# Optimization experiments

Measured on AMD Instinct MI355X. Metric: run time of the kernel, lower is better.

The kernel has to match this reference:

```python
import jax, jax.numpy as jnp
import numpy as np

NHEAD = 16
HEAD_DIM = 64
ROPE_BASE = 10000.0


def _rotate_half(x):
    # interleaved convention: pairs (x0,x1)->(-x1,x0)
    x1 = x[..., ::2]
    x2 = x[..., 1::2]
    return jnp.stack([-x2, x1], axis=-1).reshape(x.shape)


def _rope_cache(seq_len, head_dim, base):
    half = head_dim // 2
    inv_freq = 1.0 / base ** (jnp.arange(half, dtype=jnp.float32) / float(half))
    t = jnp.arange(seq_len, dtype=jnp.float32)
    freqs = jnp.einsum('i,j->ij', t, inv_freq)          # [T, half]
    emb = jnp.concatenate([freqs, freqs], axis=-1)      # [T, D] (half-half cat, matches torch source)
    return jnp.cos(emb), jnp.sin(emb)


def setup_inputs() -> dict:
    key = jax.random.key(0)
    k1, k2, k3 = jax.random.split(key, 3)
    b, t, c = 2, 2048, 1024
    x = jax.random.normal(k1, (b, t, c), dtype=jnp.float32)
    # torch nn.Linear weights: [out_features, in_features], scaled like kaiming-uniform-ish
    W_qkv = jax.random.normal(k2, (3 * c, c), dtype=jnp.float32) / np.sqrt(c)
    W_out = jax.random.normal(k3, (c, c), dtype=jnp.float32) / np.sqrt(c)
    return {"x": x, "W_qkv": W_qkv, "W_out": W_out}


def reference(x, W_qkv, W_out):
    b, t, c = x.shape
    nh, hd = NHEAD, HEAD_DIM
    qkv = x @ W_qkv.T                                   # [b, t, 3c]
    q, k, v = jnp.split(qkv, 3, axis=-1)

    def to_heads(a):
        return a.reshape(b, t, nh, hd).transpose(0, 2, 1, 3)  # [b, nh, t, hd]

    q, k, v = to_heads(q), to_heads(k), to_heads(v)
    cos, sin = _rope_cache(t, hd, ROPE_BASE)            # [t, hd]
    cos = cos.astype(q.dtype)[None, None]
    sin = sin.astype(q.dtype)[None, None]
    q = q * cos + _rotate_half(q) * sin
    k = k * cos + _rotate_half(k) * sin

    scale = 1.0 / np.sqrt(hd).astype(np.float32)
    scores = jnp.einsum('bhqd,bhkd->bhqk', q, k) * scale
    attn = jax.nn.softmax(scores, axis=-1)
    y = jnp.einsum('bhqk,bhkd->bhqd', attn, v)          # [b, nh, t, hd]
    y = y.transpose(0, 2, 1, 3).reshape(b, t, c)
    return y @ W_out.T
```

## Files before the change

### kernel.cpp

```cpp
#include <hip/hip_runtime.h>
#include <hip/hip_bf16.h>
#include <math.h>

typedef __hip_bfloat16 bf16;
typedef _Float16 f16;
typedef __attribute__((ext_vector_type(8))) short bf16x8;
typedef __attribute__((ext_vector_type(8))) _Float16 f16x8;
typedef __attribute__((ext_vector_type(4))) float f32x4;

#define MFMA_BF(a,b,c) __builtin_amdgcn_mfma_f32_16x16x32_bf16((a),(b),(c),0,0,0)
#define MFMA_F16(a,b,c) __builtin_amdgcn_mfma_f32_16x16x32_f16((a),(b),(c),0,0,0)

__device__ __forceinline__ void load_lds16(const void* g, void* l) {
  __builtin_amdgcn_global_load_lds(
      (__attribute__((address_space(1))) void*)(g),
      (__attribute__((address_space(3))) void*)(l), 16, 0, 0);
}

__device__ __forceinline__ unsigned pk_bf16(float a, float b) {
  unsigned ua = __builtin_bit_cast(unsigned, a);
  unsigned ub = __builtin_bit_cast(unsigned, b);
  ua += 0x7fffu + ((ua >> 16) & 1u);
  ub += 0x7fffu + ((ub >> 16) & 1u);
  return (ua >> 16) | (ub & 0xffff0000u);
}

__global__ void cvt_all(const float* __restrict__ x, const float* __restrict__ wq,
                        const float* __restrict__ wo, unsigned* __restrict__ xb,
                        unsigned* __restrict__ wqb, unsigned* __restrict__ wob) {
  int i = blockIdx.x * blockDim.x + threadIdx.x;
  const float* src;
  unsigned* dst;
  int off;
  if (i < 1048576) { src = x; dst = xb; off = i; }
  else if (i < 1048576 + 786432) { src = wq; dst = wqb; off = i - 1048576; }
  else { src = wo; dst = wob; off = i - (1048576 + 786432); }
  float4 v = reinterpret_cast<const float4*>(src)[off];
  uint2 u;
  u.x = pk_bf16(v.x, v.y);
  u.y = pk_bf16(v.z, v.w);
  reinterpret_cast<uint2*>(dst)[off] = u;
}

__global__ __launch_bounds__(256, 2)
void gemm_qkv(const bf16* __restrict__ A, const bf16* __restrict__ B,
              bf16* __restrict__ outq, bf16* __restrict__ outk,
              f16* __restrict__ outv) {
  __shared__ __align__(16) bf16 As[128 * 32];
  __shared__ __align__(16) bf16 Bs[128 * 32];
  __shared__ __align__(16) f16 Ts[4][32 * 72];
  const int K = 1024;
  const int tid = threadIdx.x;
  const int w = tid >> 6;
  const int lane = tid & 63;
  const int quad = lane >> 4;
  const int col = lane & 15;
  const int waveM = w >> 1;
  const int waveN = w & 1;
  const int bm = blockIdx.y * 128;
  const int bn = blockIdx.x * 128;

  f32x4 acc[4][4] = {};
  const int srow = lane >> 2;
  const int skoff = (lane & 3) * 8;

  for (int k0 = 0; k0 < K; k0 += 32) {
    __syncthreads();
#pragma unroll
    for (int p = 0; p < 2; ++p) {
      int r = p * 64 + w * 16 + srow;
      load_lds16(A + (size_t)(bm + r) * K + k0 + skoff, (char*)As + p * 4096 + w * 1024);
      load_lds16(B + (size_t)(bn + r) * K + k0 + skoff, (char*)Bs + p * 4096 + w * 1024);
    }
    __syncthreads();
    bf16x8 af[4], bfr[4];
#pragma unroll
    for (int i = 0; i < 4; ++i)
      af[i] = *reinterpret_cast<const bf16x8*>(As + (waveM * 64 + i * 16 + col) * 32 + quad * 8);
#pragma unroll
    for (int j = 0; j < 4; ++j)
      bfr[j] = *reinterpret_cast<const bf16x8*>(Bs + (waveN * 64 + j * 16 + col) * 32 + quad * 8);
#pragma unroll
    for (int i = 0; i < 4; ++i)
#pragma unroll
      for (int j = 0; j < 4; ++j)
        acc[i][j] = MFMA_BF(af[i], bfr[j], acc[i][j]);
  }

  if (bn < 2048) {
    const float NEGK = -0.4152410118f;
    const float C1 = 0.1803368799f;
    const float sgn = (col & 1) ? 1.0f : -1.0f;
#pragma unroll
    for (int j = 0; j < 4; ++j) {
      const int n0 = bn + waveN * 64 + j * 16;
      const int sel = n0 >> 10;
      const int hh = (n0 & 1023) >> 6;
      const int dd = (n0 & 63) + col;
      bf16* outp = sel ? outk : outq;
      const float post = sel ? 1.0f : C1;
      const float invf = __builtin_amdgcn_exp2f((float)((n0 & 31) + col) * NEGK);
#pragma unroll
      for (int i = 0; i < 4; ++i) {
#pragma unroll
        for (int r = 0; r < 4; ++r) {
          int m = bm + waveM * 64 + i * 16 + quad * 4 + r;
          int b = m >> 11, t = m & 2047;
          float v = acc[i][j][r];
          float partner = __shfl_xor(v, 1);
          float ang = (float)t * invf;
          float res = (v * __cosf(ang) + sgn * partner * __sinf(ang)) * post;
          outp[((size_t)(b * 16 + hh) * 2048 + t) * 64 + dd] = __float2bfloat16(res);
        }
      }
    }
  } else {
    f16* tb = &Ts[w][0];
    const int nq = bn + waveN * 64;
    const int hh = (nq & 1023) >> 6;
    const int b = bm >> 11;
    const int tbase = (bm & 2047) + waveM * 64;
    f16* dst0 = outv + (size_t)(b * 16 + hh) * 64 * 2048;
#pragma unroll
    for (int jh = 0; jh < 2; ++jh) {
#pragma unroll
      for (int j2 = 0; j2 < 2; ++j2) {
        const int j = jh * 2 + j2;
        const int dl = j2 * 16 + col;
#pragma unroll
        for (int i = 0; i < 4; ++i)
#pragma unroll
          for (int r = 0; r < 4; ++r)
            tb[dl * 72 + i * 16 + quad * 4 + r] = (f16)acc[i][j][r];
      }
      __asm__ volatile("s_waitcnt lgkmcnt(0)" ::: "memory");
      const int dl = lane >> 1;
      const int thalf = (lane & 1) * 32;
#pragma unroll
      for (int rr = 0; rr < 4; ++rr) {
        f16x8 vrow = *reinterpret_cast<const f16x8*>(tb + dl * 72 + thalf + rr * 8);
        *reinterpret_cast<f16x8*>(dst0 + (size_t)(jh * 32 + dl) * 2048 + tbase + thalf + rr * 8) = vrow;
      }
      __asm__ volatile("s_waitcnt lgkmcnt(0)" ::: "memory");
    }
  }
}

__global__ __launch_bounds__(256, 2)
void gemm_out(const bf16* __restrict__ A, const bf16* __restrict__ B,
              float* __restrict__ outf) {
  __shared__ __align__(16) bf16 As[64 * 32];
  __shared__ __align__(16) bf16 Bs[128 * 32];
  const int K = 1024;
  const int tid = threadIdx.x;
  const int w = tid >> 6;
  const int lane = tid & 63;
  const int quad = lane >> 4;
  const int col = lane & 15;
  const int bm = blockIdx.y * 64;
  const int bn = blockIdx.x * 128;

  f32x4 acc[4][2] = {};
  const int srow = lane >> 2;
  const int skoff = (lane & 3) * 8;

  for (int k0 = 0; k0 < K; k0 += 32) {
    __syncthreads();
    load_lds16(A + (size_t)(bm + w * 16 + srow) * K + k0 + skoff, (char*)As + w * 1024);
#pragma unroll
    for (int p = 0; p < 2; ++p)
      load_lds16(B + (size_t)(bn + p * 64 + w * 16 + srow) * K + k0 + skoff,
                 (char*)Bs + p * 4096 + w * 1024);
    __syncthreads();
    bf16x8 af[4], bfr[2];
#pragma unroll
    for (int i = 0; i < 4; ++i)
      af[i] = *reinterpret_cast<const bf16x8*>(As + (i * 16 + col) * 32 + quad * 8);
#pragma unroll
    for (int j = 0; j < 2; ++j)
      bfr[j] = *reinterpret_cast<const bf16x8*>(Bs + (w * 32 + j * 16 + col) * 32 + quad * 8);
#pragma unroll
    for (int i = 0; i < 4; ++i)
#pragma unroll
      for (int j = 0; j < 2; ++j)
        acc[i][j] = MFMA_BF(af[i], bfr[j], acc[i][j]);
  }

#pragma unroll
  for (int i = 0; i < 4; ++i)
#pragma unroll
    for (int j = 0; j < 2; ++j) {
      const int n0 = bn + w * 32 + j * 16;
#pragma unroll
      for (int r = 0; r < 4; ++r) {
        int m = bm + i * 16 + quad * 4 + r;
        outf[(size_t)m * 1024 + n0 + col] = acc[i][j][r];
      }
    }
}

__global__ __launch_bounds__(256, 2)
void attn_kernel(const bf16* __restrict__ qh, const bf16* __restrict__ kh,
                 const f16* __restrict__ vt, bf16* __restrict__ y) {
  __shared__ __align__(16) bf16 Ks[2][64 * 64];
  __shared__ __align__(16) f16 Vs[2][64 * 64];
  __shared__ __align__(16) f16 Ps[4][32 * 72];

  const int bh = blockIdx.y;
  const int w = threadIdx.x >> 6;
  const int lane = threadIdx.x & 63;
  const int quad = lane >> 4;
  const int col = lane & 15;

  const int qrow0 = blockIdx.x * 128 + w * 32 + col;
  bf16x8 qf[2][2];
#pragma unroll
  for (int f = 0; f < 2; ++f)
#pragma unroll
    for (int c = 0; c < 2; ++c)
      qf[f][c] = *reinterpret_cast<const bf16x8*>(
          qh + ((size_t)bh * 2048 + qrow0 + f * 16) * 64 + c * 32 + quad * 8);

  const int s8 = lane >> 3;
  const int blk = (lane & 7) ^ s8;
  const bf16* kg = kh + (size_t)bh * 2048 * 64;
  const f16* vg = vt + (size_t)bh * 64 * 2048;
  char* klds0 = (char*)&Ks[0][0] + w * 2048;
  char* vlds0 = (char*)&Vs[0][0] + w * 2048;
  const int ksrc0 = s8 * 4 + w;
  const int ksrc1 = (8 + s8) * 4 + w;
  const int vrow0 = w * 16 + s8;

  const int csw = col & 7;
  const int sw0 = (quad ^ csw) * 8;
  const int sw1 = ((quad + 4) ^ csw) * 8;
  const int rdbase = col * 64;

  f32x4 O[2][4] = {};
  float l[2][4] = {};
  f16* ps = &Ps[w][0];

  load_lds16(kg + (size_t)ksrc0 * 64 + blk * 8, klds0);
  load_lds16(kg + (size_t)ksrc1 * 64 + blk * 8, klds0 + 1024);
  load_lds16(vg + (size_t)vrow0 * 2048 + blk * 8, vlds0);
  load_lds16(vg + (size_t)(vrow0 + 8) * 2048 + blk * 8, vlds0 + 1024);

  int buf = 0;
  for (int kc = 0; kc < 2048; kc += 64) {
    __asm__ volatile("s_waitcnt vmcnt(0)" ::: "memory");
    __asm__ volatile("s_barrier" ::: "memory");
    if (kc + 64 < 2048) {
      const int nb = buf ^ 1;
      const int kn = kc + 64;
      load_lds16(kg + (size_t)(kn + ksrc0) * 64 + blk * 8, klds0 + nb * 8192);
      load_lds16(kg + (size_t)(kn + ksrc1) * 64 + blk * 8, klds0 + nb * 8192 + 1024);
      load_lds16(vg + (size_t)vrow0 * 2048 + kn + blk * 8, vlds0 + nb * 8192);
      load_lds16(vg + (size_t)(vrow0 + 8) * 2048 + kn + blk * 8, vlds0 + nb * 8192 + 1024);
    }

    const bf16* kt = &Ks[buf][0];
    const f16* vtile = &Vs[buf][0];

    f32x4 s[2][4];
#pragma unroll
    for (int t = 0; t < 4; ++t) {
      bf16x8 kf0 = *reinterpret_cast<const bf16x8*>(kt + t * 1024 + rdbase + sw0);
      bf16x8 kf1 = *reinterpret_cast<const bf16x8*>(kt + t * 1024 + rdbase + sw1);
#pragma unroll
      for (int f = 0; f < 2; ++f) {
        f32x4 a = {};
        a = MFMA_BF(qf[f][0], kf0, a);
        a = MFMA_BF(qf[f][1], kf1, a);
        s[f][t] = a;
      }
    }

#pragma unroll
    for (int f = 0; f < 2; ++f)
#pragma unroll
      for (int r = 0; r < 4; ++r) {
        float p0 = __builtin_amdgcn_exp2f(s[f][0][r]);
        float p1 = __builtin_amdgcn_exp2f(s[f][1][r]);
        float p2 = __builtin_amdgcn_exp2f(s[f][2][r]);
        float p3 = __builtin_amdgcn_exp2f(s[f][3][r]);
        l[f][r] += (p0 + p1) + (p2 + p3);
        uint2 w2;
        w2.x = __builtin_bit_cast(unsigned, __builtin_amdgcn_cvt_pkrtz(p0, p1));
        w2.y = __builtin_bit_cast(unsigned, __builtin_amdgcn_cvt_pkrtz(p2, p3));
        *reinterpret_cast<uint2*>((char*)ps + (f * 16 + quad * 4 + r) * 144 + col * 8) = w2;
      }
    __asm__ volatile("s_waitcnt lgkmcnt(0)" ::: "memory");

    f16x8 pf[2][2];
#pragma unroll
    for (int f = 0; f < 2; ++f) {
      pf[f][0] = *reinterpret_cast<const f16x8*>(ps + (f * 16 + col) * 72 + quad * 8);
      pf[f][1] = *reinterpret_cast<const f16x8*>(ps + (f * 16 + col) * 72 + 32 + quad * 8);
    }

#pragma unroll
    for (int j = 0; j < 4; ++j) {
      f16x8 vf0 = *reinterpret_cast<const f16x8*>(vtile + j * 1024 + rdbase + sw0);
      f16x8 vf1 = *reinterpret_cast<const f16x8*>(vtile + j * 1024 + rdbase + sw1);
#pragma unroll
      for (int f = 0; f < 2; ++f) {
        O[f][j] = MFMA_F16(pf[f][0], vf0, O[f][j]);
        O[f][j] = MFMA_F16(pf[f][1], vf1, O[f][j]);
      }
    }
    buf ^= 1;
  }

  const int b = bh >> 4, h = bh & 15;
#pragma unroll
  for (int f = 0; f < 2; ++f)
#pragma unroll
    for (int r = 0; r < 4; ++r) {
      float lv = l[f][r];
#pragma unroll
      for (int off = 1; off < 16; off <<= 1)
        lv += __shfl_xor(lv, off, 64);
      float inv = 1.0f / lv;
      int t = blockIdx.x * 128 + w * 32 + f * 16 + quad * 4 + r;
      size_t base = ((size_t)b * 2048 + t) * 1024 + h * 64;
#pragma unroll
      for (int j = 0; j < 4; ++j)
        y[base + j * 16 + col] = __float2bfloat16(O[f][j][r] * inv);
    }
}

extern "C" void kernel_launch(void* const* d_in, const int* in_sizes, int n_in,
                              void* d_out, int out_size, void* d_ws, size_t ws_size,
                              hipStream_t stream) {
  const float* x    = (const float*)d_in[0];
  const float* wqkv = (const float*)d_in[1];
  const float* wout = (const float*)d_in[2];
  float* out = (float*)d_out;
  char* ws = (char*)d_ws;

  bf16* xb    = (bf16*)(ws);
  bf16* wqkvb = (bf16*)(ws + (size_t)(8 << 20));
  bf16* woutb = (bf16*)(ws + (size_t)(14 << 20));
  bf16* qh    = (bf16*)(ws + (size_t)(16 << 20));
  bf16* kh    = (bf16*)(ws + (size_t)(24 << 20));
  f16*  vt    = (f16*) (ws + (size_t)(32 << 20));
  bf16* y     = (bf16*)(ws + (size_t)(40 << 20));

  cvt_all<<<8192, 256, 0, stream>>>(x, wqkv, wout,
                                    (unsigned*)xb, (unsigned*)wqkvb, (unsigned*)woutb);
  gemm_qkv<<<dim3(24, 32), 256, 0, stream>>>(xb, wqkvb, qh, kh, vt);
  attn_kernel<<<dim3(16, 32), 256, 0, stream>>>(qh, kh, vt, y);
  gemm_out<<<dim3(8, 64), 256, 0, stream>>>(y, woutb, out);
}
```

Baseline: 195.3 us.

## Split attention over two KV halves and merge partial outputs in a separate kernel

The attention kernel now splits the 2048-key range into two halves on a new grid dimension, doubling the block count. Each half writes unnormalized partial outputs in bf16 plus per-row softmax denominators to workspace, and a new merge_y kernel sums the halves and normalizes. Launch bounds go from 2 to 3 blocks per CU to raise occupancy. The goal is better CU utilisation than 512 blocks gave. The cost is an extra kernel launch, extra global traffic, and rounding unnormalized partials to bf16. Workspace regions are reused by aliasing buffers that earlier stages no longer need.

```diff
diff --git a/kernel.cpp b/kernel.cpp
--- a/kernel.cpp
+++ b/kernel.cpp
@@ -199,14 +199,17 @@
     }
 }
 
-__global__ __launch_bounds__(256, 2)
+__global__ __launch_bounds__(256, 3)
 void attn_kernel(const bf16* __restrict__ qh, const bf16* __restrict__ kh,
-                 const f16* __restrict__ vt, bf16* __restrict__ y) {
+                 const f16* __restrict__ vt, bf16* __restrict__ O1,
+                 bf16* __restrict__ O2, float* __restrict__ lw) {
   __shared__ __align__(16) bf16 Ks[2][64 * 64];
   __shared__ __align__(16) f16 Vs[2][64 * 64];
   __shared__ __align__(16) f16 Ps[4][32 * 72];
 
-  const int bh = blockIdx.y;
+  const int bh = blockIdx.z;
+  const int split = blockIdx.y;
+  const int kc0 = split << 10;
   const int w = threadIdx.x >> 6;
   const int lane = threadIdx.x & 63;
   const int quad = lane >> 4;
@@ -240,16 +243,17 @@
   float l[2][4] = {};
   f16* ps = &Ps[w][0];
 
-  load_lds16(kg + (size_t)ksrc0 * 64 + blk * 8, klds0);
-  load_lds16(kg + (size_t)ksrc1 * 64 + blk * 8, klds0 + 1024);
-  load_lds16(vg + (size_t)vrow0 * 2048 + blk * 8, vlds0);
-  load_lds16(vg + (size_t)(vrow0 + 8) * 2048 + blk * 8, vlds0 + 1024);
+  load_lds16(kg + (size_t)(kc0 + ksrc0) * 64 + blk * 8, klds0);
+  load_lds16(kg + (size_t)(kc0 + ksrc1) * 64 + blk * 8, klds0 + 1024);
+  load_lds16(vg + (size_t)vrow0 * 2048 + kc0 + blk * 8, vlds0);
+  load_lds16(vg + (size_t)(vrow0 + 8) * 2048 + kc0 + blk * 8, vlds0 + 1024);
 
   int buf = 0;
-  for (int kc = 0; kc < 2048; kc += 64) {
+  const int kend = kc0 + 1024;
+  for (int kc = kc0; kc < kend; kc += 64) {
     __asm__ volatile("s_waitcnt vmcnt(0)" ::: "memory");
     __asm__ volatile("s_barrier" ::: "memory");
-    if (kc + 64 < 2048) {
+    if (kc + 64 < kend) {
       const int nb = buf ^ 1;
       const int kn = kc + 64;
       load_lds16(kg + (size_t)(kn + ksrc0) * 64 + blk * 8, klds0 + nb * 8192);
@@ -311,6 +315,8 @@
     buf ^= 1;
   }
 
+  bf16* o_out = split ? O2 : O1;
+  float* lrow = lw + split * 65536 + bh * 2048;
   const int b = bh >> 4, h = bh & 15;
 #pragma unroll
   for (int f = 0; f < 2; ++f)
@@ -320,13 +326,48 @@
 #pragma unroll
       for (int off = 1; off < 16; off <<= 1)
         lv += __shfl_xor(lv, off, 64);
-      float inv = 1.0f / lv;
       int t = blockIdx.x * 128 + w * 32 + f * 16 + quad * 4 + r;
+      if (col == 0) lrow[t] = lv;
       size_t base = ((size_t)b * 2048 + t) * 1024 + h * 64;
 #pragma unroll
       for (int j = 0; j < 4; ++j)
-        y[base + j * 16 + col] = __float2bfloat16(O[f][j][r] * inv);
-    }
+        o_out[base + j * 16 + col] = __float2bfloat16(O[f][j][r]);
+    }
+}
+
+__global__ void merge_y(const bf16* __restrict__ O1, const bf16* __restrict__ O2,
+                        const float* __restrict__ lw, bf16* __restrict__ y) {
+  int i = blockIdx.x * blockDim.x + threadIdx.x;
+  int c8 = i & 127;
+  int t = (i >> 7) & 2047;
+  int b = i >> 18;
+  int bh = b * 16 + (c8 >> 3);
+  float inv = 1.0f / (lw[bh * 2048 + t] + lw[65536 + bh * 2048 + t]);
+  size_t off = (size_t)i * 8;
+  ushort4 a1 = *reinterpret_cast<const ushort4*>((const unsigned short*)O1 + off);
+  ushort4 a2 = *reinterpret_cast<const ushort4*>((const unsigned short*)O2 + off);
+  ushort4 b1 = *reinterpret_cast<const ushort4*>((const unsigned short*)O1 + off + 4);
+  ushort4 b2 = *reinterpret_cast<const ushort4*>((const unsigned short*)O2 + off + 4);
+  const unsigned short* u1 = &a1.x;
+  const unsigned short* u2 = &a2.x;
+  const unsigned short* v1 = &b1.x;
+  const unsigned short* v2 = &b2.x;
+  float o[8];
+#pragma unroll
+  for (int e = 0; e < 4; ++e) {
+    float s1 = __builtin_bit_cast(float, (unsigned)u1[e] << 16) +
+               __builtin_bit_cast(float, (unsigned)u2[e] << 16);
+    float s2 = __builtin_bit_cast(float, (unsigned)v1[e] << 16) +
+               __builtin_bit_cast(float, (unsigned)v2[e] << 16);
+    o[e] = s1 * inv;
+    o[e + 4] = s2 * inv;
+  }
+  uint4 res;
+  res.x = pk_bf16(o[0], o[1]);
+  res.y = pk_bf16(o[2], o[3]);
+  res.z = pk_bf16(o[4], o[5]);
+  res.w = pk_bf16(o[6], o[7]);
+  *reinterpret_cast<uint4*>((unsigned short*)y + off) = res;
 }
 
 extern "C" void kernel_launch(void* const* d_in, const int* in_sizes, int n_in,
@@ -344,11 +385,15 @@
   bf16* qh    = (bf16*)(ws + (size_t)(16 << 20));
   bf16* kh    = (bf16*)(ws + (size_t)(24 << 20));
   f16*  vt    = (f16*) (ws + (size_t)(32 << 20));
-  bf16* y     = (bf16*)(ws + (size_t)(40 << 20));
+  bf16* O1    = (bf16*)(ws + (size_t)(40 << 20));
+  bf16* O2    = (bf16*)(ws);
+  float* lw   = (float*)(ws + (size_t)(8 << 20));
+  bf16* y     = (bf16*)(ws + (size_t)(16 << 20));
 
   cvt_all<<<8192, 256, 0, stream>>>(x, wqkv, wout,
                                     (unsigned*)xb, (unsigned*)wqkvb, (unsigned*)woutb);
   gemm_qkv<<<dim3(24, 32), 256, 0, stream>>>(xb, wqkvb, qh, kh, vt);
-  attn_kernel<<<dim3(16, 32), 256, 0, stream>>>(qh, kh, vt, y);
+  attn_kernel<<<dim3(16, 2, 32), 256, 0, stream>>>(qh, kh, vt, O1, O2, lw);
+  merge_y<<<2048, 256, 0, stream>>>(O1, O2, lw, y);
   gemm_out<<<dim3(8, 64), 256, 0, stream>>>(y, woutb, out);
 }
```

After: 201.9 us. 3.4% more time.
